# Optimization experiments

Hardware: AMD Instinct MI355X
Metric: run time of the kernel (lower is better)

## Reference

```python
import jax, jax.numpy as jnp
import numpy as np

B, S, D, H, E, K = 2, 1024, 1024, 512, 16, 4  # batch, seq, hidden, expert inter, n_experts, top_k
HS = 2 * H  # shared expert inter dim = num_shared_experts * moe_inter_dim


def silu(z):
    return z * jax.nn.sigmoid(z)


def setup_inputs() -> dict:
    key = jax.random.key(0)
    ks = jax.random.split(key, 8)
    sc = lambda fan_in: 1.0 / np.sqrt(fan_in)
    x = jax.random.normal(ks[0], (B, S, D), jnp.float32)
    gate_w = jax.random.normal(ks[1], (E, D), jnp.float32) * sc(D)
    ws_in = jax.random.normal(ks[2], (D, HS), jnp.float32) * sc(D)
    vs_in = jax.random.normal(ks[3], (D, HS), jnp.float32) * sc(D)
    ws_out = jax.random.normal(ks[4], (HS, D), jnp.float32) * sc(HS)
    e_win = jax.random.normal(ks[5], (E, D, H), jnp.float32) * sc(D)
    e_vin = jax.random.normal(ks[6], (E, D, H), jnp.float32) * sc(D)
    e_wout = jax.random.normal(ks[7], (E, H, D), jnp.float32) * sc(H)
    return {"x": x, "gate_w": gate_w, "ws_in": ws_in, "vs_in": vs_in,
            "ws_out": ws_out, "e_win": e_win, "e_vin": e_vin, "e_wout": e_wout}


def reference(x, gate_w, ws_in, vs_in, ws_out, e_win, e_vin, e_wout):
    b, s, d = x.shape
    T = b * s
    xf = x.reshape(T, d)

    # --- Gate (eval path: biases buffer is zero / unused) ---
    g = jax.nn.sigmoid(xf @ gate_w.T)                      # [T, E]
    topv, topi = jax.lax.top_k(g, K)                        # [T, K]
    wn = topv / jnp.sum(topv, axis=-1, keepdims=True)       # normalized top-k weights
    # sparse combine matrix [T, E]: zero for unrouted experts -> exact same math
    # as the original per-expert masked gather/scatter loop
    combine = jnp.zeros_like(g).at[jnp.arange(T)[:, None], topi].add(wn)

    # --- Routed experts (SwiGLU), batched over experts ---
    hin = jnp.einsum('td,edh->eth', xf, e_win)              # [E, T, H]
    vin = jnp.einsum('td,edh->eth', xf, e_vin)              # [E, T, H]
    h = silu(hin) * vin * combine.T[:, :, None]             # weight before down-proj
    routed = jnp.einsum('eth,ehd->td', h, e_wout)           # [T, D]

    # --- Shared expert (SwiGLU with inter = num_shared * moe_inter) ---
    shared = (silu(xf @ ws_in) * (xf @ vs_in)) @ ws_out     # [T, D]

    return (shared + routed).reshape(b, s, d)
```

## Files before the change

### kernel.cpp

```cpp
#include <hip/hip_runtime.h>
#include <hip/hip_bf16.h>
#include <math.h>

typedef __attribute__((ext_vector_type(4))) float f32x4;
typedef __attribute__((ext_vector_type(8))) short s16x8;
typedef __hip_bfloat16 bf16;

constexpr int TOK = 2048;
constexpr int DIM = 1024;
constexpr int HID = 512;
constexpr int NE  = 16;
constexpr int NK  = 4;
constexpr int NHS = 1024;
constexpr int NPAIR = TOK * NK;

constexpr int UP_GRID = 128 + 4 * 80;
constexpr int DN_GRID = 64 + 4 * 80;

#define MFMA(a, b, c) __builtin_amdgcn_mfma_f32_16x16x32_bf16(a, b, c, 0, 0, 0)

#define GLOAD_LDS(gp, lp)                                                        \
  __builtin_amdgcn_global_load_lds(                                              \
      (const __attribute__((address_space(1))) unsigned int*)(gp),               \
      (__attribute__((address_space(3))) unsigned int*)(lp), 16, 0, 0)

template <int CH>
static __device__ __forceinline__ void stage_p(const bf16* const* rp, int k0,
                                               bf16* lds, int tid) {
  int wid = tid >> 6;
#pragma unroll
  for (int i = 0; i < CH; ++i) {
    int c = i * 512 + tid;
    int row = c >> 3;
    int slot = c & 7;
    int j = slot ^ (row & 7);
    const bf16* g = rp[i] + k0 + j * 8;
    bf16* l = lds + (size_t)(i * 512 + wid * 64) * 8;
    GLOAD_LDS(g, l);
  }
}

static __device__ __forceinline__ s16x8 frag(const bf16* lds, int row, int kc) {
  return *(const s16x8*)(lds + row * 64 + ((kc ^ (row & 7)) << 3));
}

static __device__ __forceinline__ float b2f(short u) {
  union { unsigned int i; float f; } c;
  c.i = ((unsigned int)(unsigned short)u) << 16;
  return c.f;
}

struct bf16x4 { bf16 a, b, c, d; };
struct alignas(16) bf16x8 { bf16 v[8]; };


static __device__ __forceinline__ void tr64(const float* __restrict__ src,
                                            bf16* __restrict__ dst, int R, int C,
                                            int bx, int by, float (*t)[65], int tid) {
  int r0 = by * 64, c0 = bx * 64;
#pragma unroll
  for (int i = 0; i < 4; ++i) {
    int row = i * 16 + (tid >> 4);
    int col = (tid & 15) * 4;
    float4 v = *(const float4*)(src + (size_t)(r0 + row) * C + c0 + col);
    t[row][col] = v.x; t[row][col + 1] = v.y;
    t[row][col + 2] = v.z; t[row][col + 3] = v.w;
  }
  __syncthreads();
  int c = tid >> 2;
  int rb = (tid & 3) * 16;
  bf16x8 o0, o1;
#pragma unroll
  for (int k = 0; k < 8; ++k) o0.v[k] = __float2bfloat16(t[rb + k][c]);
#pragma unroll
  for (int k = 0; k < 8; ++k) o1.v[k] = __float2bfloat16(t[rb + 8 + k][c]);
  bf16* d = dst + (size_t)(c0 + c) * R + r0 + rb;
  *(bf16x8*)d = o0;
  *(bf16x8*)(d + 8) = o1;
}

__global__ __launch_bounds__(256) void prep1(const float* __restrict__ ws_in,
                                             const float* __restrict__ vs_in,
                                             const float* __restrict__ e_win,
                                             const float* __restrict__ e_vin,
                                             bf16* __restrict__ wsinT, bf16* __restrict__ vsinT,
                                             bf16* __restrict__ ewinT, bf16* __restrict__ evinT) {
  __shared__ float t[64][65];
  int bid = blockIdx.x, tid = threadIdx.x;
  if (bid < 256) {
    tr64(ws_in, wsinT, DIM, NHS, bid & 15, bid >> 4, t, tid);
  } else if (bid < 512) {
    int b = bid - 256;
    tr64(vs_in, vsinT, DIM, NHS, b & 15, b >> 4, t, tid);
  } else if (bid < 2560) {
    int b = bid - 512, e = b >> 7; b &= 127;
    tr64(e_win + (size_t)e * DIM * HID, ewinT + (size_t)e * DIM * HID,
         DIM, HID, b & 7, b >> 3, t, tid);
  } else {
    int b = bid - 2560, e = b >> 7; b &= 127;
    tr64(e_vin + (size_t)e * DIM * HID, evinT + (size_t)e * DIM * HID,
         DIM, HID, b & 7, b >> 3, t, tid);
  }
}

__global__ __launch_bounds__(256) void prep2(const float* __restrict__ ws_out,
                                             const float* __restrict__ e_wout,
                                             bf16* __restrict__ wsoutT,
                                             bf16* __restrict__ ewoutT) {
  __shared__ float t[64][65];
  int bid = blockIdx.x, tid = threadIdx.x;
  if (bid < 256) {
    tr64(ws_out, wsoutT, NHS, DIM, bid & 15, bid >> 4, t, tid);
  } else {
    int b = bid - 256, e = b >> 7; b &= 127;
    tr64(e_wout + (size_t)e * HID * DIM, ewoutT + (size_t)e * HID * DIM,
         HID, DIM, b & 15, b >> 4, t, tid);
  }
}


__global__ __launch_bounds__(256) void gate_scores(const float* __restrict__ x,
                                                   const float* __restrict__ gw,
                                                   bf16* __restrict__ xb,
                                                   float* __restrict__ scores) {
  int lane = threadIdx.x & 63, wid = threadIdx.x >> 6;
  int t = blockIdx.x * 4 + wid;
  const float* xr = x + (size_t)t * DIM + lane * 16;
  float4 x4[4];
#pragma unroll
  for (int q = 0; q < 4; ++q) x4[q] = *(const float4*)(xr + q * 4);
  {
    bf16* xo = xb + (size_t)t * DIM + lane * 16;
#pragma unroll
    for (int q = 0; q < 4; ++q) {
      bf16x4 o{__float2bfloat16(x4[q].x), __float2bfloat16(x4[q].y),
               __float2bfloat16(x4[q].z), __float2bfloat16(x4[q].w)};
      *reinterpret_cast<bf16x4*>(xo + q * 4) = o;
    }
  }
  float s[NE];
#pragma unroll
  for (int e = 0; e < NE; ++e) {
    const float* wr_ = gw + (size_t)e * DIM + lane * 16;
    float a = 0.f;
#pragma unroll
    for (int q = 0; q < 4; ++q) {
      float4 w4 = *(const float4*)(wr_ + q * 4);
      a += x4[q].x * w4.x + x4[q].y * w4.y + x4[q].z * w4.z + x4[q].w * w4.w;
    }
    s[e] = a;
  }
#pragma unroll
  for (int e = 0; e < NE; ++e)
#pragma unroll
    for (int off = 32; off; off >>= 1) s[e] += __shfl_xor(s[e], off);
  if (lane == 0) {
#pragma unroll
    for (int e = 0; e < NE; ++e) scores[(size_t)t * NE + e] = s[e];
  }
}

__global__ __launch_bounds__(256) void topk_hist(const float* __restrict__ scores,
                                                 int* __restrict__ topi,
                                                 float* __restrict__ topw,
                                                 int* __restrict__ counts) {
  __shared__ int h[NE];
  int tid = threadIdx.x;
  int t = blockIdx.x * 256 + tid;
  if (tid < NE) h[tid] = 0;
  __syncthreads();
  float g[NE];
  const float* sr = scores + (size_t)t * NE;
#pragma unroll
  for (int q = 0; q < 4; ++q) {
    float4 v = *(const float4*)(sr + q * 4);
    g[q * 4 + 0] = 1.f / (1.f + expf(-v.x));
    g[q * 4 + 1] = 1.f / (1.f + expf(-v.y));
    g[q * 4 + 2] = 1.f / (1.f + expf(-v.z));
    g[q * 4 + 3] = 1.f / (1.f + expf(-v.w));
  }
  unsigned used = 0;
  int bi[NK]; float bv[NK];
  float sum = 0.f;
#pragma unroll
  for (int j = 0; j < NK; ++j) {
    int best = 0; float v = -1e30f;
#pragma unroll
    for (int e = 0; e < NE; ++e)
      if (!((used >> e) & 1u) && g[e] > v) { v = g[e]; best = e; }
    used |= 1u << best; bi[j] = best; bv[j] = v; sum += v;
  }
  float inv = 1.f / sum;
#pragma unroll
  for (int j = 0; j < NK; ++j) {
    topi[t * NK + j] = bi[j];
    topw[t * NK + j] = bv[j] * inv;
    atomicAdd(&h[bi[j]], 1);
  }
  __syncthreads();
  if (tid < NE) atomicAdd(&counts[tid], h[tid]);
}

__global__ __launch_bounds__(64) void route_small(const int* __restrict__ counts,
                                                  int* __restrict__ offs,
                                                  int* __restrict__ segs,
                                                  int* __restrict__ nseg,
                                                  int* __restrict__ cursor) {
  if (threadIdx.x != 0) return;
  int o = 0;
#pragma unroll
  for (int e = 0; e < NE; ++e) { offs[e] = o; cursor[e * 32] = 0; o += counts[e]; }
  int s = 0;
  for (int e = 0; e < NE; ++e)
    for (int m = 0; m < counts[e]; m += 128) segs[s++] = (e << 16) | m;
  nseg[0] = s;
}

__global__ __launch_bounds__(256) void scatter_pairs(const int* __restrict__ topi,
                                                     const float* __restrict__ topw,
                                                     const int* __restrict__ offs,
                                                     int* __restrict__ cursor,
                                                     int* __restrict__ tok_list,
                                                     float* __restrict__ w_list,
                                                     int* __restrict__ pair_slot) {
  int p = blockIdx.x * 256 + threadIdx.x;
  if (p >= NPAIR) return;
  int e = topi[p];
  int rank = atomicAdd(&cursor[e * 32], 1);
  int slot = offs[e] + rank;
  tok_list[slot] = p >> 2;
  w_list[slot] = topw[p];
  pair_slot[p] = slot;
}


__global__ __launch_bounds__(512, 4) void up_all(
    const bf16* __restrict__ xb, const bf16* __restrict__ wsinT,
    const bf16* __restrict__ vsinT, const bf16* __restrict__ ewinT,
    const bf16* __restrict__ evinT, const int* __restrict__ tok_list,
    const float* __restrict__ w_list, const int* __restrict__ counts,
    const int* __restrict__ offs, const int* __restrict__ segs,
    const int* __restrict__ nseg, bf16* __restrict__ hsb,
    bf16* __restrict__ hre) {
  int bid = blockIdx.x;
  int j = (bid & 7) * (UP_GRID / 8) + (bid >> 3);
  int nj = 128 + 4 * nseg[0];
  if (j >= nj) return;
  int tid = threadIdx.x, lane = tid & 63, wid = tid >> 6;
  int wr = wid >> 2, wc = wid & 3;

  bool is_shared = (j < 128);
  int m0, n0, cnt = TOK, off_e = 0;
  const bf16 *w1, *w2;
  if (is_shared) {
    m0 = (j >> 3) * 128; n0 = j & 7;
    w1 = wsinT; w2 = vsinT;
  } else {
    int r = j - 128;
    int sv = segs[r >> 2]; n0 = r & 3;
    int e = sv >> 16; m0 = sv & 0xffff;
    cnt = counts[e]; off_e = offs[e];
    w1 = ewinT + (size_t)e * HID * DIM;
    w2 = evinT + (size_t)e * HID * DIM;
  }

  const bf16* ap[2]; const bf16* bp[4];
#pragma unroll
  for (int i = 0; i < 2; ++i) {
    int row = (i * 512 + tid) >> 3;
    int gr = is_shared ? (m0 + row) : tok_list[off_e + min(m0 + row, cnt - 1)];
    ap[i] = xb + (size_t)gr * DIM;
  }
#pragma unroll
  for (int i = 0; i < 4; ++i) {
    int r = (i * 512 + tid) >> 3;
    int ridx = n0 * 128 + (r >> 5) * 16 + (r & 15);
    bp[i] = ((r & 16) ? w2 : w1) + (size_t)ridx * DIM;
  }

  __shared__ alignas(16) bf16 As[128 * 64], Bs[2][256 * 64];
  f32x4 acc[4][4];
  f32x4 z4 = {0.f, 0.f, 0.f, 0.f};
#pragma unroll
  for (int m = 0; m < 4; ++m)
#pragma unroll
    for (int q = 0; q < 4; ++q) acc[m][q] = z4;

  constexpr int NT = DIM / 64;
  stage_p<2>(ap, 0, As, tid);
  stage_p<4>(bp, 0, Bs[0], tid);

  for (int kt = 0; kt < NT; ++kt) {
    if (kt + 1 < NT) {
      stage_p<4>(bp, (kt + 1) * 64, Bs[(kt + 1) & 1], tid);
      asm volatile("s_waitcnt vmcnt(4)" ::: "memory");
    } else {
      asm volatile("s_waitcnt vmcnt(0)" ::: "memory");
    }
    __builtin_amdgcn_sched_barrier(0);
    __builtin_amdgcn_s_barrier();
    __builtin_amdgcn_sched_barrier(0);
    const bf16* Bc = Bs[kt & 1];
    __builtin_amdgcn_s_setprio(1);
#pragma unroll
    for (int ks = 0; ks < 2; ++ks) {
      int r16 = lane & 15, kc = (ks << 2) + (lane >> 4);
      s16x8 a[4];
#pragma unroll
      for (int m = 0; m < 4; ++m) a[m] = frag(As, wr * 64 + m * 16 + r16, kc);
#pragma unroll
      for (int q = 0; q < 4; ++q) {
        s16x8 b = frag(Bc, wc * 64 + q * 16 + r16, kc);
#pragma unroll
        for (int m = 0; m < 4; ++m) acc[m][q] = MFMA(a[m], b, acc[m][q]);
      }
    }
    __builtin_amdgcn_s_setprio(0);
    __builtin_amdgcn_sched_barrier(0);
    __builtin_amdgcn_s_barrier();
    __builtin_amdgcn_sched_barrier(0);
    if (kt + 1 < NT) stage_p<2>(ap, (kt + 1) * 64, As, tid);
  }
#pragma unroll
  for (int m = 0; m < 4; ++m)
#pragma unroll
    for (int q = 0; q < 4; q += 2) {
      int c = n0 * 128 + (wc * 2 + (q >> 1)) * 16 + (lane & 15);
#pragma unroll
      for (int i = 0; i < 4; ++i) {
        int r = wr * 64 + m * 16 + (lane >> 4) * 4 + i;
        float z = acc[m][q][i], v = acc[m][q + 1][i];
        float h = z / (1.f + __expf(-z)) * v;
        if (is_shared) {
          hsb[(size_t)(m0 + r) * NHS + c] = __float2bfloat16(h);
        } else {
          int gr = m0 + r;
          if (gr < cnt)
            hre[(size_t)(off_e + gr) * HID + c] =
                __float2bfloat16(h * w_list[off_e + gr]);
        }
      }
    }
}


__global__ __launch_bounds__(512, 4) void down_all(
    const bf16* __restrict__ hsb, const bf16* __restrict__ wsoutT,
    const bf16* __restrict__ hre, const bf16* __restrict__ ewoutT,
    const int* __restrict__ tok_list, const int* __restrict__ counts,
    const int* __restrict__ offs, const int* __restrict__ segs,
    const int* __restrict__ nseg, float* __restrict__ out,
    bf16* __restrict__ hrd) {
  int bid = blockIdx.x;
  int j = (bid & 7) * (DN_GRID / 8) + (bid >> 3);
  int nj = 64 + 4 * nseg[0];
  if (j >= nj) return;
  int tid = threadIdx.x, lane = tid & 63, wid = tid >> 6;
  int wr = wid >> 2, wc = wid & 3;

  bool is_shared = (j < 64);
  int m0, n0, cnt = TOK, off_e = 0, K, ldA, ldB;
  const bf16 *Abase, *Bbase;
  if (is_shared) {
    m0 = (j >> 2) * 128; n0 = j & 3;
    Abase = hsb; ldA = NHS; K = NHS;
    Bbase = wsoutT; ldB = NHS;
  } else {
    int r = j - 64;
    int sv = segs[r >> 2]; n0 = r & 3;
    int e = sv >> 16; m0 = sv & 0xffff;
    cnt = counts[e]; off_e = offs[e];
    Abase = hre + (size_t)off_e * HID; ldA = HID; K = HID;
    Bbase = ewoutT + (size_t)e * DIM * HID; ldB = HID;
  }

  const bf16* ap[2]; const bf16* bp[4];
#pragma unroll
  for (int i = 0; i < 2; ++i) {
    int row = (i * 512 + tid) >> 3;
    int gr = is_shared ? (m0 + row) : min(m0 + row, cnt - 1);
    ap[i] = Abase + (size_t)gr * ldA;
  }
#pragma unroll
  for (int i = 0; i < 4; ++i) {
    int r = (i * 512 + tid) >> 3;
    bp[i] = Bbase + (size_t)(n0 * 256 + r) * ldB;
  }

  __shared__ alignas(16) bf16 As[128 * 64], Bs[2][256 * 64];
  f32x4 acc[4][4];
  f32x4 z4 = {0.f, 0.f, 0.f, 0.f};
#pragma unroll
  for (int m = 0; m < 4; ++m)
#pragma unroll
    for (int q = 0; q < 4; ++q) acc[m][q] = z4;

  int NT = K / 64;
  stage_p<2>(ap, 0, As, tid);
  stage_p<4>(bp, 0, Bs[0], tid);

  for (int kt = 0; kt < NT; ++kt) {
    if (kt + 1 < NT) {
      stage_p<4>(bp, (kt + 1) * 64, Bs[(kt + 1) & 1], tid);
      asm volatile("s_waitcnt vmcnt(4)" ::: "memory");
    } else {
      asm volatile("s_waitcnt vmcnt(0)" ::: "memory");
    }
    __builtin_amdgcn_sched_barrier(0);
    __builtin_amdgcn_s_barrier();
    __builtin_amdgcn_sched_barrier(0);
    const bf16* Bc = Bs[kt & 1];
    __builtin_amdgcn_s_setprio(1);
#pragma unroll
    for (int ks = 0; ks < 2; ++ks) {
      int r16 = lane & 15, kc = (ks << 2) + (lane >> 4);
      s16x8 a[4];
#pragma unroll
      for (int m = 0; m < 4; ++m) a[m] = frag(As, wr * 64 + m * 16 + r16, kc);
#pragma unroll
      for (int q = 0; q < 4; ++q) {
        s16x8 b = frag(Bc, wc * 64 + q * 16 + r16, kc);
#pragma unroll
        for (int m = 0; m < 4; ++m) acc[m][q] = MFMA(a[m], b, acc[m][q]);
      }
    }
    __builtin_amdgcn_s_setprio(0);
    __builtin_amdgcn_sched_barrier(0);
    __builtin_amdgcn_s_barrier();
    __builtin_amdgcn_sched_barrier(0);
    if (kt + 1 < NT) stage_p<2>(ap, (kt + 1) * 64, As, tid);
  }
#pragma unroll
  for (int m = 0; m < 4; ++m)
#pragma unroll
    for (int q = 0; q < 4; ++q) {
      int c = n0 * 256 + wc * 64 + q * 16 + (lane & 15);
#pragma unroll
      for (int i = 0; i < 4; ++i) {
        int r = wr * 64 + m * 16 + (lane >> 4) * 4 + i;
        if (is_shared) {
          out[(size_t)(m0 + r) * DIM + c] = acc[m][q][i];
        } else {
          int gr = m0 + r;
          if (gr < cnt)
            hrd[(size_t)(off_e + gr) * DIM + c] = __float2bfloat16(acc[m][q][i]);
        }
      }
    }
}


__global__ __launch_bounds__(256) void finish_add(const bf16* __restrict__ hrd,
                                                  const int* __restrict__ pair_slot,
                                                  float* __restrict__ out) {
  int idx = blockIdx.x * 256 + threadIdx.x;
  int t = idx >> 7;
  int c0 = (idx & 127) * 8;
  int4 s4 = *(const int4*)(pair_slot + t * 4);
  float acc[8];
  float* o = out + (size_t)t * DIM + c0;
#pragma unroll
  for (int k = 0; k < 8; ++k) acc[k] = o[k];
  int sl[4] = {s4.x, s4.y, s4.z, s4.w};
#pragma unroll
  for (int j = 0; j < 4; ++j) {
    s16x8 v = *(const s16x8*)(hrd + (size_t)sl[j] * DIM + c0);
#pragma unroll
    for (int k = 0; k < 8; ++k) acc[k] += b2f(v[k]);
  }
#pragma unroll
  for (int k = 0; k < 8; ++k) o[k] = acc[k];
}


extern "C" void kernel_launch(void* const* d_in, const int* in_sizes, int n_in,
                              void* d_out, int out_size, void* d_ws, size_t ws_size,
                              hipStream_t stream) {
  const float* x      = (const float*)d_in[0];
  const float* gw     = (const float*)d_in[1];
  const float* ws_in  = (const float*)d_in[2];
  const float* vs_in  = (const float*)d_in[3];
  const float* ws_out = (const float*)d_in[4];
  const float* e_win  = (const float*)d_in[5];
  const float* e_vin  = (const float*)d_in[6];
  const float* e_wout = (const float*)d_in[7];
  float* out = (float*)d_out;

  char* p = (char*)d_ws;
  bf16* xb     = (bf16*)p;  p += (size_t)TOK * DIM * 2;
  bf16* wsinT  = (bf16*)p;
  bf16* wsoutT = wsinT;
  p += (size_t)NHS * DIM * 2;
  bf16* vsinT  = (bf16*)p;  p += (size_t)NHS * DIM * 2;
  bf16* hsb    = (bf16*)p;  p += (size_t)TOK * NHS * 2;
  bf16* ewinT  = (bf16*)p;
  bf16* ewoutT = ewinT;
  p += (size_t)NE * DIM * HID * 2;
  bf16* evinT  = (bf16*)p;
  bf16* hrd    = evinT;
  p += (size_t)NE * DIM * HID * 2;
  bf16* hre    = (bf16*)p;  p += (size_t)(NPAIR + 128) * HID * 2;
  int*   topi      = (int*)p;    p += (size_t)NPAIR * 4;
  float* topw      = (float*)p;  p += (size_t)NPAIR * 4;
  int*   tok_list  = (int*)p;    p += (size_t)NPAIR * 4;
  float* w_list    = (float*)p;  p += (size_t)NPAIR * 4;
  int*   pair_slot = (int*)p;    p += (size_t)NPAIR * 4;
  float* scores    = (float*)p;  p += (size_t)TOK * NE * 4;
  int*   counts    = (int*)p;    p += 64;
  int*   offs      = (int*)p;    p += 64;
  int*   cursor    = (int*)p;    p += NE * 32 * 4;
  int*   segs      = (int*)p;    p += 128 * 4;
  int*   nseg      = (int*)p;    p += 64;

  hipMemsetAsync(counts, 0, NE * sizeof(int), stream);
  gate_scores<<<TOK / 4, 256, 0, stream>>>(x, gw, xb, scores);
  topk_hist<<<TOK / 256, 256, 0, stream>>>(scores, topi, topw, counts);
  route_small<<<1, 64, 0, stream>>>(counts, offs, segs, nseg, cursor);
  scatter_pairs<<<NPAIR / 256, 256, 0, stream>>>(topi, topw, offs, cursor,
                                                 tok_list, w_list, pair_slot);

  prep1<<<4608, 256, 0, stream>>>(ws_in, vs_in, e_win, e_vin,
                                  wsinT, vsinT, ewinT, evinT);

  up_all<<<UP_GRID, 512, 0, stream>>>(xb, wsinT, vsinT, ewinT, evinT, tok_list,
                                      w_list, counts, offs, segs, nseg, hsb, hre);

  prep2<<<2304, 256, 0, stream>>>(ws_out, e_wout, wsoutT, ewoutT);

  down_all<<<DN_GRID, 512, 0, stream>>>(hsb, wsoutT, hre, ewoutT, tok_list,
                                        counts, offs, segs, nseg, out, hrd);
  finish_add<<<TOK * DIM / 8 / 256, 256, 0, stream>>>(hrd, pair_slot, out);
}
```

Measured before the change: 146.7 us.

## Fuse gate scoring into weight prep and schedule GEMM jobs per expert by XCD

```diff
diff --git a/kernel.cpp b/kernel.cpp
--- a/kernel.cpp
+++ b/kernel.cpp
@@ -14,8 +14,10 @@
 constexpr int NHS = 1024;
 constexpr int NPAIR = TOK * NK;
 
-constexpr int UP_GRID = 128 + 4 * 80;
-constexpr int DN_GRID = 64 + 4 * 80;
+constexpr int CPX_UP = 144;
+constexpr int CPX_DN = 136;
+constexpr int UP_GRID = 8 * CPX_UP;
+constexpr int DN_GRID = 8 * CPX_DN;
 
 #define MFMA(a, b, c) __builtin_amdgcn_mfma_f32_16x16x32_bf16(a, b, c, 0, 0, 0)
 
@@ -79,25 +81,64 @@
   *(bf16x8*)(d + 8) = o1;
 }
 
-__global__ __launch_bounds__(256) void prep1(const float* __restrict__ ws_in,
-                                             const float* __restrict__ vs_in,
-                                             const float* __restrict__ e_win,
-                                             const float* __restrict__ e_vin,
-                                             bf16* __restrict__ wsinT, bf16* __restrict__ vsinT,
-                                             bf16* __restrict__ ewinT, bf16* __restrict__ evinT) {
+
+__global__ __launch_bounds__(256) void prep1_gate(
+    const float* __restrict__ x, const float* __restrict__ gw,
+    bf16* __restrict__ xb, float* __restrict__ scores,
+    const float* __restrict__ ws_in, const float* __restrict__ vs_in,
+    const float* __restrict__ e_win, const float* __restrict__ e_vin,
+    bf16* __restrict__ wsinT, bf16* __restrict__ vsinT,
+    bf16* __restrict__ ewinT, bf16* __restrict__ evinT) {
   __shared__ float t[64][65];
   int bid = blockIdx.x, tid = threadIdx.x;
-  if (bid < 256) {
-    tr64(ws_in, wsinT, DIM, NHS, bid & 15, bid >> 4, t, tid);
-  } else if (bid < 512) {
-    int b = bid - 256;
+  if (bid < 512) {
+    int lane = tid & 63, wid = tid >> 6;
+    int tok = bid * 4 + wid;
+    const float* xr = x + (size_t)tok * DIM + lane * 16;
+    float4 x4[4];
+#pragma unroll
+    for (int q = 0; q < 4; ++q) x4[q] = *(const float4*)(xr + q * 4);
+    bf16* xo = xb + (size_t)tok * DIM + lane * 16;
+#pragma unroll
+    for (int q = 0; q < 4; ++q) {
+      bf16x4 o{__float2bfloat16(x4[q].x), __float2bfloat16(x4[q].y),
+               __float2bfloat16(x4[q].z), __float2bfloat16(x4[q].w)};
+      *reinterpret_cast<bf16x4*>(xo + q * 4) = o;
+    }
+    float s[NE];
+#pragma unroll
+    for (int e = 0; e < NE; ++e) {
+      const float* wr_ = gw + (size_t)e * DIM + lane * 16;
+      float a = 0.f;
+#pragma unroll
+      for (int q = 0; q < 4; ++q) {
+        float4 w4 = *(const float4*)(wr_ + q * 4);
+        a += x4[q].x * w4.x + x4[q].y * w4.y + x4[q].z * w4.z + x4[q].w * w4.w;
+      }
+      s[e] = a;
+    }
+#pragma unroll
+    for (int e = 0; e < NE; ++e)
+#pragma unroll
+      for (int off = 32; off; off >>= 1) s[e] += __shfl_xor(s[e], off);
+    if (lane == 0) {
+#pragma unroll
+      for (int e = 0; e < NE; ++e) scores[(size_t)tok * NE + e] = s[e];
+    }
+    return;
+  }
+  int b0 = bid - 512;
+  if (b0 < 256) {
+    tr64(ws_in, wsinT, DIM, NHS, b0 & 15, b0 >> 4, t, tid);
+  } else if (b0 < 512) {
+    int b = b0 - 256;
     tr64(vs_in, vsinT, DIM, NHS, b & 15, b >> 4, t, tid);
-  } else if (bid < 2560) {
-    int b = bid - 512, e = b >> 7; b &= 127;
+  } else if (b0 < 2560) {
+    int b = b0 - 512, e = b >> 7; b &= 127;
     tr64(e_win + (size_t)e * DIM * HID, ewinT + (size_t)e * DIM * HID,
          DIM, HID, b & 7, b >> 3, t, tid);
   } else {
-    int b = bid - 2560, e = b >> 7; b &= 127;
+    int b = b0 - 2560, e = b >> 7; b &= 127;
     tr64(e_vin + (size_t)e * DIM * HID, evinT + (size_t)e * DIM * HID,
          DIM, HID, b & 7, b >> 3, t, tid);
   }
@@ -118,48 +159,6 @@
   }
 }
 
-
-__global__ __launch_bounds__(256) void gate_scores(const float* __restrict__ x,
-                                                   const float* __restrict__ gw,
-                                                   bf16* __restrict__ xb,
-                                                   float* __restrict__ scores) {
-  int lane = threadIdx.x & 63, wid = threadIdx.x >> 6;
-  int t = blockIdx.x * 4 + wid;
-  const float* xr = x + (size_t)t * DIM + lane * 16;
-  float4 x4[4];
-#pragma unroll
-  for (int q = 0; q < 4; ++q) x4[q] = *(const float4*)(xr + q * 4);
-  {
-    bf16* xo = xb + (size_t)t * DIM + lane * 16;
-#pragma unroll
-    for (int q = 0; q < 4; ++q) {
-      bf16x4 o{__float2bfloat16(x4[q].x), __float2bfloat16(x4[q].y),
-               __float2bfloat16(x4[q].z), __float2bfloat16(x4[q].w)};
-      *reinterpret_cast<bf16x4*>(xo + q * 4) = o;
-    }
-  }
-  float s[NE];
-#pragma unroll
-  for (int e = 0; e < NE; ++e) {
-    const float* wr_ = gw + (size_t)e * DIM + lane * 16;
-    float a = 0.f;
-#pragma unroll
-    for (int q = 0; q < 4; ++q) {
-      float4 w4 = *(const float4*)(wr_ + q * 4);
-      a += x4[q].x * w4.x + x4[q].y * w4.y + x4[q].z * w4.z + x4[q].w * w4.w;
-    }
-    s[e] = a;
-  }
-#pragma unroll
-  for (int e = 0; e < NE; ++e)
-#pragma unroll
-    for (int off = 32; off; off >>= 1) s[e] += __shfl_xor(s[e], off);
-  if (lane == 0) {
-#pragma unroll
-    for (int e = 0; e < NE; ++e) scores[(size_t)t * NE + e] = s[e];
-  }
-}
-
 __global__ __launch_bounds__(256) void topk_hist(const float* __restrict__ scores,
                                                  int* __restrict__ topi,
                                                  float* __restrict__ topw,
@@ -203,17 +202,49 @@
 
 __global__ __launch_bounds__(64) void route_small(const int* __restrict__ counts,
                                                   int* __restrict__ offs,
-                                                  int* __restrict__ segs,
-                                                  int* __restrict__ nseg,
-                                                  int* __restrict__ cursor) {
-  if (threadIdx.x != 0) return;
-  int o = 0;
-#pragma unroll
-  for (int e = 0; e < NE; ++e) { offs[e] = o; cursor[e * 32] = 0; o += counts[e]; }
-  int s = 0;
-  for (int e = 0; e < NE; ++e)
-    for (int m = 0; m < counts[e]; m += 128) segs[s++] = (e << 16) | m;
-  nseg[0] = s;
+                                                  int* __restrict__ cursor,
+                                                  int* __restrict__ jobs_up,
+                                                  int* __restrict__ jobs_dn) {
+  __shared__ int nseg_s[NE], off_s[NE];
+  int t = threadIdx.x;
+  if (t == 0) {
+    int o = 0;
+    for (int e = 0; e < NE; ++e) { off_s[e] = o; o += counts[e]; }
+  }
+  __syncthreads();
+  if (t < NE) {
+    offs[t] = off_s[t];
+    cursor[t * 32] = 0;
+    nseg_s[t] = (counts[t] + 127) >> 7;
+  }
+  __syncthreads();
+  if (t < 16) {
+    int g = t, chunk = g & 7, base = (g >> 3) * 8;
+    for (int w = 0; w < 8; ++w) {
+      int m = (g >> 2) * 4 + (w >> 1);
+      int n0 = (g & 3) * 2 + (w & 1);
+      jobs_up[chunk * CPX_UP + base + w] = 0x40000000 | (m << 4) | n0;
+    }
+  } else if (t < 32) {
+    int e = t - 16, chunk = e & 7;
+    int base = 16 + ((e >= 8) ? 4 * nseg_s[e - 8] : 0);
+    for (int s = 0; s < nseg_s[e]; ++s)
+      for (int n = 0; n < 4; ++n)
+        jobs_up[chunk * CPX_UP + base + s * 4 + n] = (e << 8) | (s << 4) | n;
+  } else if (t < 40) {
+    int g = t - 32, chunk = g;
+    for (int w = 0; w < 8; ++w) {
+      int m = (g >> 1) * 4 + (w >> 1);
+      int n0 = (g & 1) * 2 + (w & 1);
+      jobs_dn[chunk * CPX_DN + w] = 0x40000000 | (m << 4) | n0;
+    }
+  } else if (t < 56) {
+    int e = t - 40, chunk = e & 7;
+    int base = 8 + ((e >= 8) ? 4 * nseg_s[e - 8] : 0);
+    for (int s = 0; s < nseg_s[e]; ++s)
+      for (int n = 0; n < 4; ++n)
+        jobs_dn[chunk * CPX_DN + base + s * 4 + n] = (e << 8) | (s << 4) | n;
+  }
 }
 
 __global__ __launch_bounds__(256) void scatter_pairs(const int* __restrict__ topi,
@@ -239,26 +270,23 @@
     const bf16* __restrict__ vsinT, const bf16* __restrict__ ewinT,
     const bf16* __restrict__ evinT, const int* __restrict__ tok_list,
     const float* __restrict__ w_list, const int* __restrict__ counts,
-    const int* __restrict__ offs, const int* __restrict__ segs,
-    const int* __restrict__ nseg, bf16* __restrict__ hsb,
-    bf16* __restrict__ hre) {
+    const int* __restrict__ offs, const int* __restrict__ jobs_up,
+    bf16* __restrict__ hsb, bf16* __restrict__ hre) {
   int bid = blockIdx.x;
-  int j = (bid & 7) * (UP_GRID / 8) + (bid >> 3);
-  int nj = 128 + 4 * nseg[0];
-  if (j >= nj) return;
+  int jv = jobs_up[(bid & 7) * CPX_UP + (bid >> 3)];
+  if (jv < 0) return;
   int tid = threadIdx.x, lane = tid & 63, wid = tid >> 6;
   int wr = wid >> 2, wc = wid & 3;
 
-  bool is_shared = (j < 128);
+  bool is_shared = (jv & 0x40000000) != 0;
   int m0, n0, cnt = TOK, off_e = 0;
   const bf16 *w1, *w2;
   if (is_shared) {
-    m0 = (j >> 3) * 128; n0 = j & 7;
+    m0 = ((jv >> 4) & 15) * 128; n0 = jv & 15;
     w1 = wsinT; w2 = vsinT;
   } else {
-    int r = j - 128;
-    int sv = segs[r >> 2]; n0 = r & 3;
-    int e = sv >> 16; m0 = sv & 0xffff;
+    int e = (jv >> 8) & 15;
+    m0 = ((jv >> 4) & 15) * 128; n0 = jv & 15;
     cnt = counts[e]; off_e = offs[e];
     w1 = ewinT + (size_t)e * HID * DIM;
     w2 = evinT + (size_t)e * HID * DIM;
@@ -348,27 +376,24 @@
     const bf16* __restrict__ hsb, const bf16* __restrict__ wsoutT,
     const bf16* __restrict__ hre, const bf16* __restrict__ ewoutT,
     const int* __restrict__ tok_list, const int* __restrict__ counts,
-    const int* __restrict__ offs, const int* __restrict__ segs,
-    const int* __restrict__ nseg, float* __restrict__ out,
-    bf16* __restrict__ hrd) {
+    const int* __restrict__ offs, const int* __restrict__ jobs_dn,
+    float* __restrict__ out, bf16* __restrict__ hrd) {
   int bid = blockIdx.x;
-  int j = (bid & 7) * (DN_GRID / 8) + (bid >> 3);
-  int nj = 64 + 4 * nseg[0];
-  if (j >= nj) return;
+  int jv = jobs_dn[(bid & 7) * CPX_DN + (bid >> 3)];
+  if (jv < 0) return;
   int tid = threadIdx.x, lane = tid & 63, wid = tid >> 6;
   int wr = wid >> 2, wc = wid & 3;
 
-  bool is_shared = (j < 64);
+  bool is_shared = (jv & 0x40000000) != 0;
   int m0, n0, cnt = TOK, off_e = 0, K, ldA, ldB;
   const bf16 *Abase, *Bbase;
   if (is_shared) {
-    m0 = (j >> 2) * 128; n0 = j & 3;
+    m0 = ((jv >> 4) & 15) * 128; n0 = jv & 15;
     Abase = hsb; ldA = NHS; K = NHS;
     Bbase = wsoutT; ldB = NHS;
   } else {
-    int r = j - 64;
-    int sv = segs[r >> 2]; n0 = r & 3;
-    int e = sv >> 16; m0 = sv & 0xffff;
+    int e = (jv >> 8) & 15;
+    m0 = ((jv >> 4) & 15) * 128; n0 = jv & 15;
     cnt = counts[e]; off_e = offs[e];
     Abase = hre + (size_t)off_e * HID; ldA = HID; K = HID;
     Bbase = ewoutT + (size_t)e * DIM * HID; ldB = HID;
@@ -509,25 +534,26 @@
   int*   counts    = (int*)p;    p += 64;
   int*   offs      = (int*)p;    p += 64;
   int*   cursor    = (int*)p;    p += NE * 32 * 4;
-  int*   segs      = (int*)p;    p += 128 * 4;
-  int*   nseg      = (int*)p;    p += 64;
+  int*   jobs_up   = (int*)p;    p += UP_GRID * 4;
+  int*   jobs_dn   = (int*)p;    p += DN_GRID * 4;
 
   hipMemsetAsync(counts, 0, NE * sizeof(int), stream);
-  gate_scores<<<TOK / 4, 256, 0, stream>>>(x, gw, xb, scores);
+  hipMemsetAsync(jobs_up, 0xFF, UP_GRID * sizeof(int), stream);
+  hipMemsetAsync(jobs_dn, 0xFF, DN_GRID * sizeof(int), stream);
+
+  prep1_gate<<<5120, 256, 0, stream>>>(x, gw, xb, scores, ws_in, vs_in,
+                                       e_win, e_vin, wsinT, vsinT, ewinT, evinT);
   topk_hist<<<TOK / 256, 256, 0, stream>>>(scores, topi, topw, counts);
-  route_small<<<1, 64, 0, stream>>>(counts, offs, segs, nseg, cursor);
+  route_small<<<1, 64, 0, stream>>>(counts, offs, cursor, jobs_up, jobs_dn);
   scatter_pairs<<<NPAIR / 256, 256, 0, stream>>>(topi, topw, offs, cursor,
                                                  tok_list, w_list, pair_slot);
 
-  prep1<<<4608, 256, 0, stream>>>(ws_in, vs_in, e_win, e_vin,
-                                  wsinT, vsinT, ewinT, evinT);
-
   up_all<<<UP_GRID, 512, 0, stream>>>(xb, wsinT, vsinT, ewinT, evinT, tok_list,
-                                      w_list, counts, offs, segs, nseg, hsb, hre);
+                                      w_list, counts, offs, jobs_up, hsb, hre);
 
   prep2<<<2304, 256, 0, stream>>>(ws_out, e_wout, wsoutT, ewoutT);
 
   down_all<<<DN_GRID, 512, 0, stream>>>(hsb, wsoutT, hre, ewoutT, tok_list,
-                                        counts, offs, segs, nseg, out, hrd);
+                                        counts, offs, jobs_dn, out, hrd);
   finish_add<<<TOK * DIM / 8 / 256, 256, 0, stream>>>(hrd, pair_slot, out);
 }
```

After: 134.2 us, median of 2. -8.5%, faster.
